# Kernel tuning notes

Measured on AMD Instinct MI355X. Metric: run time of the kernel, lower is better.

## Reference

```python
import jax, jax.numpy as jnp
import numpy as np

B, N = 4, 2048
NFEAT, NHID, NHEADS, NCLASS = 512, 64, 4, 64
ALPHA = 0.2  # leaky relu negative slope
AVG_DEG = 32.0


def setup_inputs() -> dict:
    key = jax.random.key(0)
    ks = jax.random.split(key, 6)
    x = jax.random.normal(ks[0], (B, N, NFEAT), jnp.float32)
    # sparse binary adjacency (~AVG_DEG neighbors/node) + self-loops so rowsums > 0
    adj = jax.random.bernoulli(ks[1], AVG_DEG / N, (N, N)).astype(jnp.float32)
    adj = jnp.maximum(adj, jnp.eye(N, dtype=jnp.float32))
    W1 = jax.random.normal(ks[2], (NHEADS, NFEAT, NHID), jnp.float32) * (1.0 / np.sqrt(NFEAT))
    a1 = jax.random.normal(ks[3], (NHEADS, 2 * NHID), jnp.float32) * 0.1
    W2 = jax.random.normal(ks[4], (NHEADS * NHID, NCLASS), jnp.float32) * (1.0 / np.sqrt(NHEADS * NHID))
    a2 = jax.random.normal(ks[5], (2 * NCLASS,), jnp.float32) * 0.1
    return {"x": x, "adj": adj, "W1": W1, "a1": a1, "W2": W2, "a2": a2}


def reference(x, adj, W1, a1, W2, a2):
    # Dropout layers run in eval mode (identity) for a deterministic reference.
    # --- multi-head SpGraphAttentionLayer, concat=True ---
    h = jnp.einsum('bnf,hfd->bhnd', x, W1)                      # [B,H,N,D]
    s_src = jnp.einsum('bhnd,hd->bhn', h, a1[:, :NHID])
    s_dst = jnp.einsum('bhnd,hd->bhn', h, a1[:, NHID:])
    # pyGAT sparse layer: edge_e = exp(-leakyrelu(a . [h_i || h_j])), masked by adj
    e = jnp.exp(-jax.nn.leaky_relu(s_src[..., :, None] + s_dst[..., None, :], ALPHA)) * adj  # [B,H,N,N]
    num = jnp.einsum('bhnm,bhmd->bhnd', e, h)
    den = jnp.sum(e, axis=-1, keepdims=True)
    h1 = jax.nn.elu(num / den)                                  # concat=True -> elu inside layer
    h1 = jnp.transpose(h1, (0, 2, 1, 3)).reshape(B, N, NHEADS * NHID)  # head concat
    # --- output SpGraphAttentionLayer, concat=False ---
    g = h1 @ W2                                                 # [B,N,C]
    t_src = g @ a2[:NCLASS]
    t_dst = g @ a2[NCLASS:]
    e2 = jnp.exp(-jax.nn.leaky_relu(t_src[..., :, None] + t_dst[..., None, :], ALPHA)) * adj  # [B,N,N]
    out = jnp.einsum('bnm,bmd->bnd', e2, g) / jnp.sum(e2, axis=-1, keepdims=True)
    return jax.nn.elu(out)                                      # outer F.elu in SpGAT.forward
```

## Files before the change

### kernel.cpp

```cpp
#include <hip/hip_runtime.h>
#include <hip/hip_bf16.h>

constexpr int B_ = 4, N_ = 2048, NFEAT = 512, NHID = 64, NHEADS = 4, NCLASS = 64;
constexpr int MAXDEG = 128;
#define LRELU_ALPHA 0.2f

typedef __attribute__((ext_vector_type(8))) short short8;
typedef __attribute__((ext_vector_type(4))) float f32x4;

__device__ __forceinline__ unsigned short f2bf_rne(float f) {
  unsigned int u = __float_as_uint(f);
  unsigned int r = (u + 0x7FFFu + ((u >> 16) & 1u)) >> 16;
  return (unsigned short)r;
}
__device__ __forceinline__ float bf2f(unsigned short h) {
  return __uint_as_float(((unsigned int)h) << 16);
}

__global__ __launch_bounds__(256) void build_adj_kernel(
    const float* __restrict__ adj, int* __restrict__ nbr, int* __restrict__ deg) {
  int n = blockIdx.x;
  int tid = threadIdx.x;
  __shared__ int cnt;
  if (tid == 0) cnt = 0;
  __syncthreads();
  for (int m = tid; m < N_; m += 256) {
    bool nz = adj[(size_t)n * N_ + m] != 0.0f;
    unsigned long long mask = __ballot(nz);
    int lane = tid & 63;
    int num = __popcll(mask);
    if (num) {
      int base = 0;
      if (lane == 0) base = atomicAdd(&cnt, num);
      base = __shfl(base, 0);
      if (nz) {
        int pos = base + __popcll(mask & ((1ull << lane) - 1ull));
        if (pos < MAXDEG) nbr[n * MAXDEG + pos] = m;
      }
    }
  }
  __syncthreads();
  if (tid == 0) deg[n] = cnt < MAXDEG ? cnt : MAXDEG;
}

__global__ __launch_bounds__(256) void prep_x_kernel(
    const float* __restrict__ x, unsigned short* __restrict__ xhi,
    unsigned short* __restrict__ xlo) {
  size_t idx = ((size_t)blockIdx.x * 256 + threadIdx.x) * 8;
  float4 v0 = *(const float4*)&x[idx];
  float4 v1 = *(const float4*)&x[idx + 4];
  float v[8] = {v0.x, v0.y, v0.z, v0.w, v1.x, v1.y, v1.z, v1.w};
  short8 sh, sl;
#pragma unroll
  for (int j = 0; j < 8; ++j) {
    unsigned short hi = f2bf_rne(v[j]);
    sh[j] = (short)hi;
    sl[j] = (short)f2bf_rne(v[j] - bf2f(hi));
  }
  *(short8*)&xhi[idx] = sh;
  *(short8*)&xlo[idx] = sl;
}

template <int KK>
__global__ __launch_bounds__(256) void prep_w_kernel(
    const float* __restrict__ W, unsigned short* __restrict__ wth,
    unsigned short* __restrict__ wtl) {
  __shared__ float ts[64][65];
  int h = blockIdx.y, k0 = blockIdx.x * 64;
  int tid = threadIdx.x;
  int kr = tid >> 2, nc = (tid & 3) * 16;
  const float* src = W + ((size_t)h * KK + k0 + kr) * 64 + nc;
#pragma unroll
  for (int j = 0; j < 4; ++j)
    *(float4*)&ts[kr][nc + 4 * j] = *(const float4*)(src + 4 * j);
  __syncthreads();
  int n = tid >> 2, kc = (tid & 3) * 16;
  short8 h0, h1v, l0, l1v;
#pragma unroll
  for (int j = 0; j < 8; ++j) {
    float a = ts[kc + j][n];
    float b = ts[kc + 8 + j][n];
    unsigned short ah = f2bf_rne(a), bh = f2bf_rne(b);
    h0[j] = (short)ah; h1v[j] = (short)bh;
    l0[j] = (short)f2bf_rne(a - bf2f(ah));
    l1v[j] = (short)f2bf_rne(b - bf2f(bh));
  }
  size_t o = ((size_t)h * 64 + n) * KK + k0 + kc;
  *(short8*)&wth[o]     = h0;
  *(short8*)&wth[o + 8] = h1v;
  *(short8*)&wtl[o]     = l0;
  *(short8*)&wtl[o + 8] = l1v;
}

template <int K, int MODE>
__global__ __launch_bounds__(256) void gemm_mfma_kernel(
    const unsigned short* __restrict__ Xh, const unsigned short* __restrict__ Xl,
    const unsigned short* __restrict__ Wth, const unsigned short* __restrict__ Wtl,
    const float* __restrict__ avec, float* __restrict__ Y,
    float* __restrict__ so_src, float* __restrict__ so_dst) {
  __shared__ unsigned short xsh[64][72], xsl[64][72], wsh[64][72], wsl[64][72];
  int tid = threadIdx.x;
  int w = tid >> 6, l = tid & 63;
  int row0 = blockIdx.x * 64;
  int head = blockIdx.y;
  const unsigned short* xh = Xh + (size_t)row0 * K;
  const unsigned short* xl = Xl + (size_t)row0 * K;
  const unsigned short* wh = Wth + (size_t)head * 64 * K;
  const unsigned short* wl = Wtl + (size_t)head * 64 * K;
  const float* av = avec + head * 128;

  int sr = tid >> 2;
  int sc = (tid & 3) * 16;

  f32x4 acc[4];
#pragma unroll
  for (int nt = 0; nt < 4; ++nt) acc[nt] = (f32x4){0.f, 0.f, 0.f, 0.f};

  for (int k0 = 0; k0 < K; k0 += 64) {
    {
      const unsigned short* s0 = xh + (size_t)sr * K + k0 + sc;
      const unsigned short* s1 = xl + (size_t)sr * K + k0 + sc;
      const unsigned short* s2 = wh + (size_t)sr * K + k0 + sc;
      const unsigned short* s3 = wl + (size_t)sr * K + k0 + sc;
      *(short8*)&xsh[sr][sc]     = *(const short8*)s0;
      *(short8*)&xsh[sr][sc + 8] = *(const short8*)(s0 + 8);
      *(short8*)&xsl[sr][sc]     = *(const short8*)s1;
      *(short8*)&xsl[sr][sc + 8] = *(const short8*)(s1 + 8);
      *(short8*)&wsh[sr][sc]     = *(const short8*)s2;
      *(short8*)&wsh[sr][sc + 8] = *(const short8*)(s2 + 8);
      *(short8*)&wsl[sr][sc]     = *(const short8*)s3;
      *(short8*)&wsl[sr][sc + 8] = *(const short8*)(s3 + 8);
    }
    __syncthreads();
#pragma unroll
    for (int ks = 0; ks < 2; ++ks) {
      int ko = ks * 32 + (l >> 4) * 8;
      int ar = 16 * w + (l & 15);
      short8 ah = *(const short8*)&xsh[ar][ko];
      short8 al = *(const short8*)&xsl[ar][ko];
#pragma unroll
      for (int nt = 0; nt < 4; ++nt) {
        int br = 16 * nt + (l & 15);
        short8 bh = *(const short8*)&wsh[br][ko];
        short8 bl = *(const short8*)&wsl[br][ko];
        acc[nt] = __builtin_amdgcn_mfma_f32_16x16x32_bf16(ah, bh, acc[nt], 0, 0, 0);
        acc[nt] = __builtin_amdgcn_mfma_f32_16x16x32_bf16(ah, bl, acc[nt], 0, 0, 0);
        acc[nt] = __builtin_amdgcn_mfma_f32_16x16x32_bf16(al, bh, acc[nt], 0, 0, 0);
      }
    }
    __syncthreads();
  }

  int col = (l & 15);
#pragma unroll
  for (int nt = 0; nt < 4; ++nt) {
#pragma unroll
    for (int j = 0; j < 4; ++j) {
      int r = 16 * w + (l >> 4) * 4 + j;
      size_t gr = row0 + r;
      if (MODE == 0)
        Y[gr * (NHEADS * 64) + head * 64 + 16 * nt + col] = acc[nt][j];
      else
        Y[gr * 64 + 16 * nt + col] = acc[nt][j];
    }
  }
  float aS[4], aD[4];
#pragma unroll
  for (int nt = 0; nt < 4; ++nt) {
    aS[nt] = av[16 * nt + col];
    aD[nt] = av[64 + 16 * nt + col];
  }
  float s1[4] = {0.f, 0.f, 0.f, 0.f}, s2[4] = {0.f, 0.f, 0.f, 0.f};
#pragma unroll
  for (int nt = 0; nt < 4; ++nt)
#pragma unroll
    for (int j = 0; j < 4; ++j) {
      s1[j] = fmaf(acc[nt][j], aS[nt], s1[j]);
      s2[j] = fmaf(acc[nt][j], aD[nt], s2[j]);
    }
#pragma unroll
  for (int off = 1; off < 16; off <<= 1) {
#pragma unroll
    for (int j = 0; j < 4; ++j) {
      s1[j] += __shfl_xor(s1[j], off);
      s2[j] += __shfl_xor(s2[j], off);
    }
  }
  if (col == 0) {
#pragma unroll
    for (int j = 0; j < 4; ++j) {
      int r = 16 * w + (l >> 4) * 4 + j;
      int gr = row0 + r;
      size_t si;
      if (MODE == 0) {
        int b = gr >> 11, n = gr & (N_ - 1);
        si = (size_t)(b * NHEADS + head) * N_ + n;
      } else {
        si = gr;
      }
      so_src[si] = s1[j];
      so_dst[si] = s2[j];
    }
  }
}

template <int RS>
__device__ __forceinline__ float sparse_agg(
    const float* __restrict__ plane, const float* __restrict__ sdb,
    const int* __restrict__ nb, int dg, float ss, int lane) {
  float acc0 = 0.f, acc1 = 0.f, den0 = 0.f, den1 = 0.f;
  int k = 0;
  for (; k + 8 <= dg; k += 8) {
    int m[8];
    float sv[8], hv[8];
#pragma unroll
    for (int j = 0; j < 8; ++j) m[j] = nb[k + j];
#pragma unroll
    for (int j = 0; j < 8; ++j) sv[j] = sdb[m[j]];
#pragma unroll
    for (int j = 0; j < 8; ++j) hv[j] = plane[(size_t)m[j] * RS + lane];
#pragma unroll
    for (int j = 0; j < 8; ++j) {
      float s = ss + sv[j];
      float lr = s > 0.f ? s : LRELU_ALPHA * s;
      float ev = __expf(-lr);
      if (j & 1) { den1 += ev; acc1 = fmaf(ev, hv[j], acc1); }
      else       { den0 += ev; acc0 = fmaf(ev, hv[j], acc0); }
    }
  }
  for (; k < dg; ++k) {
    int m = nb[k];
    float s = ss + sdb[m];
    float lr = s > 0.f ? s : LRELU_ALPHA * s;
    float ev = __expf(-lr);
    den0 += ev;
    acc0 = fmaf(ev, plane[(size_t)m * RS + lane], acc0);
  }
  return (acc0 + acc1) / (den0 + den1);
}

__global__ __launch_bounds__(256) void attn1_kernel(
    const float* __restrict__ Hm, const float* __restrict__ ssrc,
    const float* __restrict__ sdst, const int* __restrict__ nbr,
    const int* __restrict__ deg, unsigned short* __restrict__ h1h,
    unsigned short* __restrict__ h1l) {
  int bn = blockIdx.x;
  int n = bn & (N_ - 1), b = bn >> 11;
  int w = threadIdx.x >> 6;
  int lane = threadIdx.x & 63;
  __shared__ int lds_nbr[MAXDEG];
  int dg = deg[n];
  for (int k = threadIdx.x; k < dg; k += 256) lds_nbr[k] = nbr[n * MAXDEG + k];
  __syncthreads();
  int bh = b * NHEADS + w;
  float ss = ssrc[(size_t)bh * N_ + n];
  const float* sdb = sdst + (size_t)bh * N_;
  const float* plane = Hm + (size_t)b * N_ * (NHEADS * 64) + w * 64;
  float o = sparse_agg<NHEADS * 64>(plane, sdb, lds_nbr, dg, ss, lane);
  o = o > 0.f ? o : expm1f(o);
  unsigned short hi = f2bf_rne(o);
  size_t oi = (size_t)bn * (NHEADS * NHID) + w * 64 + lane;
  h1h[oi] = hi;
  h1l[oi] = f2bf_rne(o - bf2f(hi));
}

__global__ __launch_bounds__(256) void attn2_kernel(
    const float* __restrict__ G, const float* __restrict__ tsrc,
    const float* __restrict__ tdst, const int* __restrict__ nbr,
    const int* __restrict__ deg, float* __restrict__ out) {
  int w = threadIdx.x >> 6, lane = threadIdx.x & 63;
  int gr = blockIdx.x * 4 + w;
  int n = gr & (N_ - 1);
  int b = gr >> 11;
  float o = sparse_agg<64>(G + (size_t)b * N_ * 64, tdst + (size_t)b * N_,
                           nbr + n * MAXDEG, deg[n], tsrc[gr], lane);
  out[(size_t)gr * 64 + lane] = o > 0.f ? o : expm1f(o);
}

extern "C" void kernel_launch(void* const* d_in, const int* in_sizes, int n_in,
                              void* d_out, int out_size, void* d_ws, size_t ws_size,
                              hipStream_t stream) {
  const float* x   = (const float*)d_in[0];
  const float* adj = (const float*)d_in[1];
  const float* W1  = (const float*)d_in[2];
  const float* a1  = (const float*)d_in[3];
  const float* W2  = (const float*)d_in[4];
  const float* a2  = (const float*)d_in[5];
  float* out = (float*)d_out;

  char* ws = (char*)d_ws;
  float* h    = (float*)ws; ws += (size_t)B_ * N_ * 256 * 4;
  float* g    = (float*)ws; ws += (size_t)B_ * N_ * 64 * 4;
  float* ssrc = (float*)ws; ws += (size_t)B_ * NHEADS * N_ * 4;
  float* sdst = (float*)ws; ws += (size_t)B_ * NHEADS * N_ * 4;
  float* tsrc = (float*)ws; ws += (size_t)B_ * N_ * 4;
  float* tdst = (float*)ws; ws += (size_t)B_ * N_ * 4;
  int*   nbr  = (int*)ws;   ws += (size_t)N_ * MAXDEG * 4;
  int*   deg  = (int*)ws;   ws += (size_t)N_ * 4;
  ws = (char*)(((size_t)ws + 255) & ~(size_t)255);
  unsigned short* xhi  = (unsigned short*)ws; ws += (size_t)B_ * N_ * NFEAT * 2;
  unsigned short* xlo  = (unsigned short*)ws; ws += (size_t)B_ * N_ * NFEAT * 2;
  unsigned short* wt1h = (unsigned short*)ws; ws += (size_t)NHEADS * 64 * NFEAT * 2;
  unsigned short* wt1l = (unsigned short*)ws; ws += (size_t)NHEADS * 64 * NFEAT * 2;
  unsigned short* wt2h = (unsigned short*)ws; ws += (size_t)64 * 256 * 2;
  unsigned short* wt2l = (unsigned short*)ws; ws += (size_t)64 * 256 * 2;
  unsigned short* h1h  = (unsigned short*)ws; ws += (size_t)B_ * N_ * 256 * 2;
  unsigned short* h1l  = (unsigned short*)ws; ws += (size_t)B_ * N_ * 256 * 2;

  build_adj_kernel<<<N_, 256, 0, stream>>>(adj, nbr, deg);
  prep_x_kernel<<<(B_ * N_ * NFEAT) / (256 * 8), 256, 0, stream>>>(x, xhi, xlo);
  prep_w_kernel<NFEAT><<<dim3(NFEAT / 64, NHEADS), 256, 0, stream>>>(W1, wt1h, wt1l);
  prep_w_kernel<256><<<dim3(256 / 64, 1), 256, 0, stream>>>(W2, wt2h, wt2l);
  gemm_mfma_kernel<NFEAT, 0><<<dim3(B_ * N_ / 64, NHEADS), 256, 0, stream>>>(
      xhi, xlo, wt1h, wt1l, a1, h, ssrc, sdst);
  attn1_kernel<<<B_ * N_, 256, 0, stream>>>(h, ssrc, sdst, nbr, deg, h1h, h1l);
  gemm_mfma_kernel<256, 1><<<dim3(B_ * N_ / 64, 1), 256, 0, stream>>>(
      h1h, h1l, wt2h, wt2l, a2, g, tsrc, tdst);
  attn2_kernel<<<B_ * N_ / 4, 256, 0, stream>>>(g, tsrc, tdst, nbr, deg, out);
}
```

Baseline: 149.2 us.

## Fuse x bf16 split into GEMM load and merge prep kernels

Drops the separate prep_x pass that wrote hi/lo bf16 copies of x to global memory. The first GEMM now reads fp32 x directly and splits it into hi/lo bf16 while staging into shared memory. The adjacency build and both weight-prep kernels are merged into one launch, selected by block index. This removes a full read/write pass over x (about 16MB in, 16MB out) and two launches. In exchange, each of the four head blocks re-reads and re-converts the same x tile, so fp32 x traffic into the GEMM doubles relative to bf16 and the conversion work is repeated per head.

```diff
diff --git a/kernel.cpp b/kernel.cpp
--- a/kernel.cpp
+++ b/kernel.cpp
@@ -17,94 +17,79 @@
   return __uint_as_float(((unsigned int)h) << 16);
 }
 
-__global__ __launch_bounds__(256) void build_adj_kernel(
-    const float* __restrict__ adj, int* __restrict__ nbr, int* __restrict__ deg) {
-  int n = blockIdx.x;
+__global__ __launch_bounds__(256) void prep_kernel(
+    const float* __restrict__ adj, int* __restrict__ nbr, int* __restrict__ deg,
+    const float* __restrict__ W1, unsigned short* __restrict__ wt1h,
+    unsigned short* __restrict__ wt1l, const float* __restrict__ W2,
+    unsigned short* __restrict__ wt2h, unsigned short* __restrict__ wt2l) {
+  __shared__ float ts[64][65];
+  __shared__ int cnt;
+  int bid = blockIdx.x;
   int tid = threadIdx.x;
-  __shared__ int cnt;
-  if (tid == 0) cnt = 0;
-  __syncthreads();
-  for (int m = tid; m < N_; m += 256) {
-    bool nz = adj[(size_t)n * N_ + m] != 0.0f;
-    unsigned long long mask = __ballot(nz);
-    int lane = tid & 63;
-    int num = __popcll(mask);
-    if (num) {
-      int base = 0;
-      if (lane == 0) base = atomicAdd(&cnt, num);
-      base = __shfl(base, 0);
-      if (nz) {
-        int pos = base + __popcll(mask & ((1ull << lane) - 1ull));
-        if (pos < MAXDEG) nbr[n * MAXDEG + pos] = m;
+  if (bid < N_) {
+    int n = bid;
+    if (tid == 0) cnt = 0;
+    __syncthreads();
+    for (int m = tid; m < N_; m += 256) {
+      bool nz = adj[(size_t)n * N_ + m] != 0.0f;
+      unsigned long long mask = __ballot(nz);
+      int lane = tid & 63;
+      int num = __popcll(mask);
+      if (num) {
+        int base = 0;
+        if (lane == 0) base = atomicAdd(&cnt, num);
+        base = __shfl(base, 0);
+        if (nz) {
+          int pos = base + __popcll(mask & ((1ull << lane) - 1ull));
+          if (pos < MAXDEG) nbr[n * MAXDEG + pos] = m;
+        }
       }
     }
-  }
-  __syncthreads();
-  if (tid == 0) deg[n] = cnt < MAXDEG ? cnt : MAXDEG;
-}
-
-__global__ __launch_bounds__(256) void prep_x_kernel(
-    const float* __restrict__ x, unsigned short* __restrict__ xhi,
-    unsigned short* __restrict__ xlo) {
-  size_t idx = ((size_t)blockIdx.x * 256 + threadIdx.x) * 8;
-  float4 v0 = *(const float4*)&x[idx];
-  float4 v1 = *(const float4*)&x[idx + 4];
-  float v[8] = {v0.x, v0.y, v0.z, v0.w, v1.x, v1.y, v1.z, v1.w};
-  short8 sh, sl;
-#pragma unroll
-  for (int j = 0; j < 8; ++j) {
-    unsigned short hi = f2bf_rne(v[j]);
-    sh[j] = (short)hi;
-    sl[j] = (short)f2bf_rne(v[j] - bf2f(hi));
-  }
-  *(short8*)&xhi[idx] = sh;
-  *(short8*)&xlo[idx] = sl;
-}
-
-template <int KK>
-__global__ __launch_bounds__(256) void prep_w_kernel(
-    const float* __restrict__ W, unsigned short* __restrict__ wth,
-    unsigned short* __restrict__ wtl) {
-  __shared__ float ts[64][65];
-  int h = blockIdx.y, k0 = blockIdx.x * 64;
-  int tid = threadIdx.x;
-  int kr = tid >> 2, nc = (tid & 3) * 16;
-  const float* src = W + ((size_t)h * KK + k0 + kr) * 64 + nc;
-#pragma unroll
-  for (int j = 0; j < 4; ++j)
-    *(float4*)&ts[kr][nc + 4 * j] = *(const float4*)(src + 4 * j);
-  __syncthreads();
-  int n = tid >> 2, kc = (tid & 3) * 16;
-  short8 h0, h1v, l0, l1v;
-#pragma unroll
-  for (int j = 0; j < 8; ++j) {
-    float a = ts[kc + j][n];
-    float b = ts[kc + 8 + j][n];
-    unsigned short ah = f2bf_rne(a), bh = f2bf_rne(b);
-    h0[j] = (short)ah; h1v[j] = (short)bh;
-    l0[j] = (short)f2bf_rne(a - bf2f(ah));
-    l1v[j] = (short)f2bf_rne(b - bf2f(bh));
-  }
-  size_t o = ((size_t)h * 64 + n) * KK + k0 + kc;
-  *(short8*)&wth[o]     = h0;
-  *(short8*)&wth[o + 8] = h1v;
-  *(short8*)&wtl[o]     = l0;
-  *(short8*)&wtl[o + 8] = l1v;
+    __syncthreads();
+    if (tid == 0) deg[n] = cnt < MAXDEG ? cnt : MAXDEG;
+  } else {
+    int wk = bid - N_;
+    const float* W;
+    unsigned short *wth, *wtl;
+    int KK, h, k0;
+    if (wk < 32) { W = W1; wth = wt1h; wtl = wt1l; KK = 512; h = wk >> 3; k0 = (wk & 7) * 64; }
+    else { wk -= 32; W = W2; wth = wt2h; wtl = wt2l; KK = 256; h = 0; k0 = wk * 64; }
+    int kr = tid >> 2, nc = (tid & 3) * 16;
+    const float* src = W + ((size_t)h * KK + k0 + kr) * 64 + nc;
+#pragma unroll
+    for (int j = 0; j < 4; ++j)
+      *(float4*)&ts[kr][nc + 4 * j] = *(const float4*)(src + 4 * j);
+    __syncthreads();
+    int n = tid >> 2, kc = (tid & 3) * 16;
+    short8 h0, h1v, l0, l1v;
+#pragma unroll
+    for (int j = 0; j < 8; ++j) {
+      float a = ts[kc + j][n];
+      float b = ts[kc + 8 + j][n];
+      unsigned short ah = f2bf_rne(a), bh = f2bf_rne(b);
+      h0[j] = (short)ah; h1v[j] = (short)bh;
+      l0[j] = (short)f2bf_rne(a - bf2f(ah));
+      l1v[j] = (short)f2bf_rne(b - bf2f(bh));
+    }
+    size_t o = ((size_t)h * 64 + n) * KK + k0 + kc;
+    *(short8*)&wth[o]     = h0;
+    *(short8*)&wth[o + 8] = h1v;
+    *(short8*)&wtl[o]     = l0;
+    *(short8*)&wtl[o + 8] = l1v;
+  }
 }
 
 template <int K, int MODE>
 __global__ __launch_bounds__(256) void gemm_mfma_kernel(
-    const unsigned short* __restrict__ Xh, const unsigned short* __restrict__ Xl,
-    const unsigned short* __restrict__ Wth, const unsigned short* __restrict__ Wtl,
-    const float* __restrict__ avec, float* __restrict__ Y,
-    float* __restrict__ so_src, float* __restrict__ so_dst) {
+    const float* __restrict__ Xf, const unsigned short* __restrict__ Xh,
+    const unsigned short* __restrict__ Xl, const unsigned short* __restrict__ Wth,
+    const unsigned short* __restrict__ Wtl, const float* __restrict__ avec,
+    float* __restrict__ Y, float* __restrict__ so_src, float* __restrict__ so_dst) {
   __shared__ unsigned short xsh[64][72], xsl[64][72], wsh[64][72], wsl[64][72];
   int tid = threadIdx.x;
   int w = tid >> 6, l = tid & 63;
   int row0 = blockIdx.x * 64;
   int head = blockIdx.y;
-  const unsigned short* xh = Xh + (size_t)row0 * K;
-  const unsigned short* xl = Xl + (size_t)row0 * K;
   const unsigned short* wh = Wth + (size_t)head * 64 * K;
   const unsigned short* wl = Wtl + (size_t)head * 64 * K;
   const float* av = avec + head * 128;
@@ -117,15 +102,39 @@
   for (int nt = 0; nt < 4; ++nt) acc[nt] = (f32x4){0.f, 0.f, 0.f, 0.f};
 
   for (int k0 = 0; k0 < K; k0 += 64) {
-    {
-      const unsigned short* s0 = xh + (size_t)sr * K + k0 + sc;
-      const unsigned short* s1 = xl + (size_t)sr * K + k0 + sc;
-      const unsigned short* s2 = wh + (size_t)sr * K + k0 + sc;
-      const unsigned short* s3 = wl + (size_t)sr * K + k0 + sc;
+    if (MODE == 0) {
+      const float* s0 = Xf + (size_t)(row0 + sr) * K + k0 + sc;
+      float4 f0 = ((const float4*)s0)[0];
+      float4 f1 = ((const float4*)s0)[1];
+      float4 f2 = ((const float4*)s0)[2];
+      float4 f3 = ((const float4*)s0)[3];
+      float v[16] = {f0.x, f0.y, f0.z, f0.w, f1.x, f1.y, f1.z, f1.w,
+                     f2.x, f2.y, f2.z, f2.w, f3.x, f3.y, f3.z, f3.w};
+      short8 hi0, hi1, lo0, lo1;
+#pragma unroll
+      for (int j = 0; j < 8; ++j) {
+        unsigned short hh = f2bf_rne(v[j]);
+        hi0[j] = (short)hh;
+        lo0[j] = (short)f2bf_rne(v[j] - bf2f(hh));
+        unsigned short hh1 = f2bf_rne(v[8 + j]);
+        hi1[j] = (short)hh1;
+        lo1[j] = (short)f2bf_rne(v[8 + j] - bf2f(hh1));
+      }
+      *(short8*)&xsh[sr][sc]     = hi0;
+      *(short8*)&xsh[sr][sc + 8] = hi1;
+      *(short8*)&xsl[sr][sc]     = lo0;
+      *(short8*)&xsl[sr][sc + 8] = lo1;
+    } else {
+      const unsigned short* s0 = Xh + (size_t)(row0 + sr) * K + k0 + sc;
+      const unsigned short* s1 = Xl + (size_t)(row0 + sr) * K + k0 + sc;
       *(short8*)&xsh[sr][sc]     = *(const short8*)s0;
       *(short8*)&xsh[sr][sc + 8] = *(const short8*)(s0 + 8);
       *(short8*)&xsl[sr][sc]     = *(const short8*)s1;
       *(short8*)&xsl[sr][sc + 8] = *(const short8*)(s1 + 8);
+    }
+    {
+      const unsigned short* s2 = wh + (size_t)sr * K + k0 + sc;
+      const unsigned short* s3 = wl + (size_t)sr * K + k0 + sc;
       *(short8*)&wsh[sr][sc]     = *(const short8*)s2;
       *(short8*)&wsh[sr][sc + 8] = *(const short8*)(s2 + 8);
       *(short8*)&wsl[sr][sc]     = *(const short8*)s3;
@@ -298,8 +307,6 @@
   int*   nbr  = (int*)ws;   ws += (size_t)N_ * MAXDEG * 4;
   int*   deg  = (int*)ws;   ws += (size_t)N_ * 4;
   ws = (char*)(((size_t)ws + 255) & ~(size_t)255);
-  unsigned short* xhi  = (unsigned short*)ws; ws += (size_t)B_ * N_ * NFEAT * 2;
-  unsigned short* xlo  = (unsigned short*)ws; ws += (size_t)B_ * N_ * NFEAT * 2;
   unsigned short* wt1h = (unsigned short*)ws; ws += (size_t)NHEADS * 64 * NFEAT * 2;
   unsigned short* wt1l = (unsigned short*)ws; ws += (size_t)NHEADS * 64 * NFEAT * 2;
   unsigned short* wt2h = (unsigned short*)ws; ws += (size_t)64 * 256 * 2;
@@ -307,14 +314,12 @@
   unsigned short* h1h  = (unsigned short*)ws; ws += (size_t)B_ * N_ * 256 * 2;
   unsigned short* h1l  = (unsigned short*)ws; ws += (size_t)B_ * N_ * 256 * 2;
 
-  build_adj_kernel<<<N_, 256, 0, stream>>>(adj, nbr, deg);
-  prep_x_kernel<<<(B_ * N_ * NFEAT) / (256 * 8), 256, 0, stream>>>(x, xhi, xlo);
-  prep_w_kernel<NFEAT><<<dim3(NFEAT / 64, NHEADS), 256, 0, stream>>>(W1, wt1h, wt1l);
-  prep_w_kernel<256><<<dim3(256 / 64, 1), 256, 0, stream>>>(W2, wt2h, wt2l);
+  prep_kernel<<<N_ + 32 + 4, 256, 0, stream>>>(adj, nbr, deg, W1, wt1h, wt1l,
+                                               W2, wt2h, wt2l);
   gemm_mfma_kernel<NFEAT, 0><<<dim3(B_ * N_ / 64, NHEADS), 256, 0, stream>>>(
-      xhi, xlo, wt1h, wt1l, a1, h, ssrc, sdst);
+      x, nullptr, nullptr, wt1h, wt1l, a1, h, ssrc, sdst);
   attn1_kernel<<<B_ * N_, 256, 0, stream>>>(h, ssrc, sdst, nbr, deg, h1h, h1l);
   gemm_mfma_kernel<256, 1><<<dim3(B_ * N_ / 64, 1), 256, 0, stream>>>(
-      h1h, h1l, wt2h, wt2l, a2, g, tsrc, tdst);
+      nullptr, h1h, h1l, wt2h, wt2l, a2, g, tsrc, tdst);
   attn2_kernel<<<B_ * N_ / 4, 256, 0, stream>>>(g, tsrc, tdst, nbr, deg, out);
 }
```

After: 144.9 us. 1.03x faster.
